# Kernel optimization log

Hardware: AMD Instinct MI355X
Metric: run time of the kernel (lower is better)

## Reference

```python
import jax, jax.numpy as jnp
import numpy as np

HIDDEN = 128   # hidden_dim == input_dim (embedding feeds LSTMCell directly)
OUT = 200000   # output_dim: item catalog size
T = 64         # num_timesteps
K = 50         # num_recommendations
HIST = 200     # length of user history x


def setup_inputs() -> dict:
    key = jax.random.key(0)
    ks = jax.random.split(key, 6)
    s = 0.02
    return {
        "x": jax.random.randint(ks[0], (HIST,), 1, OUT + 1),  # 1-indexed items
        "embed_table": jax.random.normal(ks[1], (OUT, HIDDEN), jnp.float32) * s,
        "W_ih": jax.random.normal(ks[2], (4 * HIDDEN, HIDDEN), jnp.float32) * s,
        "W_hh": jax.random.normal(ks[3], (4 * HIDDEN, HIDDEN), jnp.float32) * s,
        "b_ih": jnp.zeros((4 * HIDDEN,), jnp.float32),
        "b_hh": jnp.zeros((4 * HIDDEN,), jnp.float32),
        "W_out": jax.random.normal(ks[4], (OUT, HIDDEN), jnp.float32) * s,
        "b_out": jnp.zeros((OUT,), jnp.float32),
    }


def reference(x, embed_table, W_ih, W_hh, b_ih, b_hh, W_out, b_out):
    # Faithful translation of RecModel.forward with prev_a_hat=None, prev_feedback=None.
    def step(carry, i):
        h, c, mask, a_hat, feedback = carry
        # at i==0 the embedding input is forced to zeros (feedback starts at 0 anyway)
        emb = jnp.where(i > 0, embed_table[a_hat] * feedback.astype(jnp.float32), 0.0)
        # LSTMCell: gates order (input, forget, cell, output) as in torch
        gates = W_ih @ emb + b_ih + W_hh @ h + b_hh
        ig, fg, gg, og = jnp.split(gates, 4)
        c_new = jax.nn.sigmoid(fg) * c + jax.nn.sigmoid(ig) * jnp.tanh(gg)
        h_new = jax.nn.sigmoid(og) * jnp.tanh(c_new)
        probs = jax.nn.softmax(W_out @ h_new + b_out)  # Softmax(dim=0) on [OUT]
        masked = probs * mask
        _, top_items = jax.lax.top_k(masked, K)
        hit = jnp.isin(top_items + 1, x)               # x is 1-indexed
        any_hit = jnp.any(hit)
        first_hit = top_items[jnp.argmax(hit)]         # first intersecting item
        a_new = jnp.where(any_hit, first_hit, top_items[0]).astype(jnp.int32)
        fb_new = jnp.where(any_hit, 1, -1).astype(jnp.int32)
        mask_new = mask.at[a_new].set(0.0)
        return (h_new, c_new, mask_new, a_new, fb_new), (a_new, fb_new, masked)

    init = (
        jnp.zeros((HIDDEN,), jnp.float32),
        jnp.zeros((HIDDEN,), jnp.float32),
        jnp.ones((OUT,), jnp.float32),
        jnp.array(0, jnp.int32),
        jnp.array(0, jnp.int32),
    )
    _, (a_hats, feedbacks, masked_probs) = jax.lax.scan(step, init, jnp.arange(T))
    return a_hats, feedbacks, masked_probs
```

## Files before the change

### kernel.cpp

```cpp
#include <hip/hip_runtime.h>
#include <stdint.h>

#define OUTN   200000
#define HID    128
#define NSTEP  64
#define KTOP   50
#define NBINS  1024
#define CAP    4096
#define NBLK   256
#define NTHR   512
#define NWRD   6250

__device__ __forceinline__ float dot128f(const float* __restrict__ w, const float* __restrict__ h){
  const float4* w4 = (const float4*)w;
  float acc = 0.f;
  #pragma unroll
  for (int k=0;k<32;k++){
    float4 q = w4[k];
    const float* hp = h + k*4;
    acc += q.x*hp[0] + q.y*hp[1] + q.z*hp[2] + q.w*hp[3];
  }
  return acc;
}

__device__ __forceinline__ int binOf(float l, float rlo, float rsc){
  float b = (l - rlo) * rsc;
  b = fminf(fmaxf(b, 0.f), (float)(NBINS-1));
  return (int)b;
}

__device__ __forceinline__ void blockRed5(float& mx, float& mn, float& a, float& b, float& c,
                                          int tid, float* sm ){
  #pragma unroll
  for (int o=32;o;o>>=1){
    mx=fmaxf(mx,__shfl_xor(mx,o)); mn=fminf(mn,__shfl_xor(mn,o));
    a+=__shfl_xor(a,o); b+=__shfl_xor(b,o); c+=__shfl_xor(c,o);
  }
  __syncthreads();
  if ((tid&63)==0){ int w=tid>>6; sm[w*5+0]=mx; sm[w*5+1]=mn; sm[w*5+2]=a; sm[w*5+3]=b; sm[w*5+4]=c; }
  __syncthreads();
  int nw = blockDim.x>>6;
  if (tid==0){
    for (int k=1;k<nw;k++){
      sm[0]=fmaxf(sm[0],sm[k*5+0]); sm[1]=fminf(sm[1],sm[k*5+1]);
      sm[2]+=sm[k*5+2]; sm[3]+=sm[k*5+3]; sm[4]+=sm[k*5+4];
    }
  }
  __syncthreads();
  mx=sm[0]; mn=sm[1]; a=sm[2]; b=sm[3]; c=sm[4];
}

__device__ __forceinline__ void blockRedPair(float& p, int& i, int tid, float* smp, int* smi){
  __syncthreads();
  #pragma unroll
  for (int o=32;o;o>>=1){
    float p2=__shfl_xor(p,o); int i2=__shfl_xor(i,o);
    if (p2>p || (p2==p && i2<i)){ p=p2; i=i2; }
  }
  if ((tid&63)==0){ smp[tid>>6]=p; smi[tid>>6]=i; }
  __syncthreads();
  if (tid==0){
    for (int k=1;k<8;k++){
      if (smp[k]>smp[0] || (smp[k]==smp[0] && smi[k]<smi[0])){ smp[0]=smp[k]; smi[0]=smi[k]; }
    }
  }
  __syncthreads();
  p=smp[0]; i=smi[0];
}

__device__ __forceinline__ int blockRedSum(int v, int tid, int* smi){
  __syncthreads();
  #pragma unroll
  for (int o=32;o;o>>=1) v += __shfl_xor(v,o);
  if ((tid&63)==0) smi[tid>>6]=v;
  __syncthreads();
  if (tid==0){ int s=0; for(int k=0;k<8;k++) s+=smi[k]; smi[0]=s; }
  __syncthreads();
  return smi[0];
}

__device__ __forceinline__ void histSelect(unsigned* histL, unsigned* csum, int tid, int K, int* outp){
  int base = NBINS - 2*(tid+1);
  csum[tid] = histL[base] + histL[base+1];
  __syncthreads();
  for (int off=1; off<NTHR; off<<=1){
    unsigned add = (tid>=off) ? csum[tid-off] : 0u;
    __syncthreads();
    csum[tid] += add;
    __syncthreads();
  }
  unsigned pre = (tid==0)?0u:csum[tid-1];
  if (csum[tid] >= (unsigned)K && pre < (unsigned)K){
    unsigned run = pre; int bs = base;
    for (int b=base+1; b>=base; --b){
      run += histL[b];
      if (run >= (unsigned)K){ bs=b; break; }
    }
    outp[0]=bs; outp[1]=(int)run;
  }
  __syncthreads();
}

extern "C" __global__ void k_init(const int* __restrict__ x,
                                  const float* __restrict__ b_ih, const float* __restrict__ b_hh,
                                  unsigned* mask_bits, unsigned* inx_bits, unsigned* hist_g,
                                  unsigned* gcount, float* rparams, float* h_ws, float* c_ws)
{
  int tid = threadIdx.x;
  for (int i=tid;i<NWRD;i+=1024){ mask_bits[i]=0xFFFFFFFFu; inx_bits[i]=0u; }
  for (int i=tid;i<NBINS;i+=1024) hist_g[i]=0u;
  if (tid==0){ *gcount=0u; rparams[0]=0.f; rparams[1]=0.f; }
  if (tid<HID){
    float ig=b_ih[tid]       +b_hh[tid];
    float gg=b_ih[tid+2*HID] +b_hh[tid+2*HID];
    float og=b_ih[tid+3*HID] +b_hh[tid+3*HID];
    float si=1.f/(1.f+expf(-ig)), so=1.f/(1.f+expf(-og));
    float cn=si*tanhf(gg);
    c_ws[tid]=cn; h_ws[tid]=so*tanhf(cn);
  }
  __syncthreads();
  if (tid<200){
    int v = x[tid]-1;
    if (v>=0 && v<OUTN) atomicOr(&inx_bits[v>>5], 1u<<(v&31));
  }
}

extern "C" __global__ void __launch_bounds__(NTHR) k_logits(
    const float* __restrict__ W_out, const float* __restrict__ b_out,
    const unsigned* __restrict__ mask_bits, const float* __restrict__ h_ws,
    const float* __restrict__ rparams,
    float* __restrict__ l_ws, unsigned* __restrict__ hist_g, float* __restrict__ partials)
{
  __shared__ float    h_l[HID];
  __shared__ unsigned hl[NBINS];
  __shared__ float    smf[48];
  int tid=threadIdx.x, bid=blockIdx.x;
  if (tid<HID) h_l[tid]=h_ws[tid];
  for (int i=tid;i<NBINS;i+=NTHR) hl[i]=0u;
  __syncthreads();
  const float rlo=rparams[0], rsc=rparams[1];
  int start = bid*781 + (bid<64 ? bid : 64);
  int cnt   = 781 + (bid<64 ? 1 : 0);
  float mx=-3e38f, mn=3e38f, se=0.f, sl=0.f, sl2=0.f;
  for (int j=tid;j<cnt;j+=NTHR){
    int row = start+j;
    float l = dot128f(W_out+(size_t)row*HID, h_l) + b_out[row];
    l_ws[row]=l;
    se += expf(l)-1.f; sl += l; sl2 += l*l;
    if ((mask_bits[row>>5]>>(row&31))&1u){
      mx=fmaxf(mx,l); mn=fminf(mn,l);
      atomicAdd(&hl[binOf(l,rlo,rsc)],1u);
    }
  }
  blockRed5(mx,mn,se,sl,sl2,tid,smf);
  if (tid==0){ float* p=&partials[bid*8]; p[0]=mx;p[1]=mn;p[2]=se;p[3]=sl;p[4]=sl2; }
  for (int i=tid;i<NBINS;i+=NTHR){ unsigned v=hl[i]; if (v) atomicAdd(&hist_g[i],v); }
}

extern "C" __global__ void __launch_bounds__(NTHR) k_emit(
    const float* __restrict__ l_ws, const unsigned* __restrict__ mask_bits,
    const unsigned* __restrict__ hist_g, const float* __restrict__ partials,
    const float* __restrict__ rparams,
    float* __restrict__ out, unsigned* __restrict__ cand, unsigned* __restrict__ gcount,
    int t)
{
  __shared__ unsigned hl[NBINS];
  __shared__ unsigned csum[NTHR];
  __shared__ float    smf[48];
  __shared__ int      s_sel[2];
  int tid=threadIdx.x, bid=blockIdx.x;
  float mx=-3e38f,mn=3e38f,se=0.f,sl=0.f,sl2=0.f;
  if (tid<NBLK){ const float* p=&partials[tid*8]; mx=p[0];mn=p[1];se=p[2];sl=p[3];sl2=p[4]; }
  for (int i=tid;i<NBINS;i+=NTHR) hl[i]=hist_g[i];
  blockRed5(mx,mn,se,sl,sl2,tid,smf);
  const float invS = 1.f/(2.0e5f + se);
  histSelect(hl,csum,tid,KTOP,s_sel);
  const int bstar=s_sel[0];
  const float rlo=rparams[0], rsc=rparams[1];
  const bool doComp = (s_sel[1]<=CAP) && (rsc>0.f);
  float* orow = out + 2*NSTEP + (size_t)t*OUTN;
  int start = bid*781 + (bid<64 ? bid : 64);
  int cnt   = 781 + (bid<64 ? 1 : 0);
  for (int j=tid;j<cnt;j+=NTHR){
    int row = start+j;
    float l = l_ws[row];
    bool m = (mask_bits[row>>5]>>(row&31))&1u;
    orow[row] = m ? expf(l)*invS : 0.f;
    if (doComp && m && binOf(l,rlo,rsc)>=bstar){
      unsigned pos = atomicAdd(gcount,1u);
      if (pos<CAP) cand[pos]=(unsigned)row;
    }
  }
}

extern "C" __global__ void __launch_bounds__(NTHR) k_select(
    const float* __restrict__ emb_t,
    const float* __restrict__ W_ih, const float* __restrict__ W_hh,
    const float* __restrict__ b_ih, const float* __restrict__ b_hh,
    const float* __restrict__ l_ws, const float* __restrict__ partials,
    unsigned* mask_bits, const unsigned* __restrict__ inx_bits,
    unsigned* hist_g, unsigned* cand, unsigned* gcount,
    float* rparams, float* h_ws, float* c_ws,
    float* __restrict__ out, int t)
{
  __shared__ unsigned hl[NBINS];
  __shared__ unsigned csum[NTHR];
  __shared__ float    smf[48];
  __shared__ float    smp[8];
  __shared__ int      smi[8];
  __shared__ int      s_sel[2];
  __shared__ int      s_nc, s_cnt;
  __shared__ float    emb_l[HID], h_l[HID], gates[4*HID];
  int tid=threadIdx.x;

  float mx=-3e38f,mn=3e38f,se=0.f,sl=0.f,sl2=0.f;
  if (tid<NBLK){ const float* p=&partials[tid*8]; mx=p[0];mn=p[1];se=p[2];sl=p[3];sl2=p[4]; }
  for (int i=tid;i<NBINS;i+=NTHR) hl[i]=hist_g[i];
  blockRed5(mx,mn,se,sl,sl2,tid,smf);
  const float gmax=mx, gmin=mn, slg=sl, sl2g=sl2;
  histSelect(hl,csum,tid,KTOP,s_sel);
  const float rsc=rparams[1];
  const bool doComp = (s_sel[1]<=CAP) && (rsc>0.f);
  int nc = doComp ? (int)*gcount : 0;
  bool ok = doComp && nc>=KTOP && nc<=CAP;

  if (!ok){
    if (gmin >= gmax){
      if (tid==0){
        int c=0;
        for (int i=0;i<OUTN && c<KTOP;i++)
          if ((mask_bits[i>>5]>>(i&31))&1u) cand[c++]=(unsigned)i;
        s_nc=c;
      }
    } else {
      for (int i=tid;i<NBINS;i+=NTHR) hl[i]=0u;
      __syncthreads();
      const float sc2 = (float)NBINS/(gmax-gmin);
      for (int i=tid;i<OUTN;i+=NTHR)
        if ((mask_bits[i>>5]>>(i&31))&1u)
          atomicAdd(&hl[binOf(l_ws[i],gmin,sc2)],1u);
      __syncthreads();
      histSelect(hl,csum,tid,KTOP,s_sel);
      int b2=s_sel[0], c2=s_sel[1];
      if (c2<=CAP){
        if (tid==0) s_cnt=0;
        __syncthreads();
        for (int i=tid;i<OUTN;i+=NTHR){
          if ((mask_bits[i>>5]>>(i&31))&1u && binOf(l_ws[i],gmin,sc2)>=b2){
            int p=atomicAdd(&s_cnt,1);
            if (p<CAP) cand[p]=(unsigned)i;
          }
        }
        __syncthreads();
        if (tid==0) s_nc = (s_cnt<CAP ? s_cnt : CAP);
      } else {
        if (tid==0){
          int c=0;
          for (int i=0;i<OUTN && c<KTOP;i++)
            if (((mask_bits[i>>5]>>(i&31))&1u) && binOf(l_ws[i],gmin,sc2)>=b2) cand[c++]=(unsigned)i;
          s_nc=c;
        }
      }
    }
    __syncthreads();
    nc = s_nc;
  }

  float bp=-3.4e38f; int bi=0x7fffffff;
  float hp=-3.4e38f; int hidx=0x7fffffff;
  for (int j=tid;j<nc;j+=NTHR){
    int idx=(int)cand[j];
    float l=l_ws[idx];
    if (l>bp || (l==bp && idx<bi)){ bp=l; bi=idx; }
    if (((inx_bits[idx>>5]>>(idx&31))&1u) && (l>hp || (l==hp && idx<hidx))){ hp=l; hidx=idx; }
  }
  blockRedPair(bp,bi,tid,smp,smi);
  blockRedPair(hp,hidx,tid,smp,smi);
  int a, fb;
  if (hidx != 0x7fffffff){
    int cnt=0;
    for (int j=tid;j<nc;j+=NTHR){
      int idx=(int)cand[j];
      float l=l_ws[idx];
      cnt += (l>hp || (l==hp && idx<hidx)) ? 1 : 0;
    }
    cnt = blockRedSum(cnt,tid,smi);
    if (cnt < KTOP){ a=hidx; fb=1; } else { a=bi; fb=-1; }
  } else { a=bi; fb=-1; }
  if (a<0 || a>=OUTN) a=0;

  if (tid==0){
    out[t]       = (float)a;
    out[NSTEP+t] = (float)fb;
    atomicAnd(&mask_bits[a>>5], ~(1u<<(a&31)));
  }

  if (tid<HID){
    h_l[tid]  = h_ws[tid];
    emb_l[tid]= emb_t[(size_t)a*HID+tid] * (float)fb;
  }
  __syncthreads();
  float g = dot128f(W_ih+(size_t)tid*HID, emb_l) + dot128f(W_hh+(size_t)tid*HID, h_l)
          + b_ih[tid] + b_hh[tid];
  gates[tid]=g;
  __syncthreads();
  if (tid<HID){
    float ig=gates[tid], fg=gates[tid+HID], gg=gates[tid+2*HID], og=gates[tid+3*HID];
    float si=1.f/(1.f+expf(-ig)), sf=1.f/(1.f+expf(-fg)), so=1.f/(1.f+expf(-og));
    float cn=sf*c_ws[tid]+si*tanhf(gg);
    float hn=so*tanhf(cn);
    c_ws[tid]=cn; h_ws[tid]=hn;
  }

  for (int i=tid;i<NBINS;i+=NTHR) hist_g[i]=0u;
  if (tid==0){
    *gcount=0u;
    float mean=slg/2.0e5f;
    float var =sl2g/2.0e5f - mean*mean;
    float sg  =sqrtf(fmaxf(var,0.f));
    rparams[0]=gmax-24.f*sg;
    rparams[1]=(sg>0.f)?((float)NBINS/(32.f*sg)):0.f;
  }
}

extern "C" void kernel_launch(void* const* d_in, const int* in_sizes, int n_in,
                              void* d_out, int out_size, void* d_ws, size_t ws_size,
                              hipStream_t stream)
{
  const int*   x    = (const int*)d_in[0];
  const float* emb  = (const float*)d_in[1];
  const float* Wih  = (const float*)d_in[2];
  const float* Whh  = (const float*)d_in[3];
  const float* bih  = (const float*)d_in[4];
  const float* bhh  = (const float*)d_in[5];
  const float* Wout = (const float*)d_in[6];
  const float* bout = (const float*)d_in[7];
  float* out = (float*)d_out;

  char* ws = (char*)d_ws;
  float*    l_ws      = (float*)(ws + 0);
  float*    partials  = (float*)(ws + 800000);
  unsigned* mask_bits = (unsigned*)(ws + 808192);
  unsigned* inx_bits  = (unsigned*)(ws + 833280);
  unsigned* hist_g    = (unsigned*)(ws + 858368);
  unsigned* cand      = (unsigned*)(ws + 862464);
  unsigned* gcount    = (unsigned*)(ws + 878848);
  float*    rparams   = (float*)(ws + 879104);
  float*    h_ws      = (float*)(ws + 879360);
  float*    c_ws      = (float*)(ws + 879872);

  hipLaunchKernelGGL(k_init, dim3(1), dim3(1024), 0, stream,
                     x, bih, bhh, mask_bits, inx_bits, hist_g, gcount, rparams, h_ws, c_ws);

  for (int t=0; t<NSTEP; ++t){
    hipLaunchKernelGGL(k_logits, dim3(NBLK), dim3(NTHR), 0, stream,
                       Wout, bout, mask_bits, h_ws, rparams, l_ws, hist_g, partials);
    hipLaunchKernelGGL(k_emit, dim3(NBLK), dim3(NTHR), 0, stream,
                       l_ws, mask_bits, hist_g, partials, rparams, out, cand, gcount, t);
    hipLaunchKernelGGL(k_select, dim3(1), dim3(NTHR), 0, stream,
                       emb, Wih, Whh, bih, bhh, l_ws, partials, mask_bits, inx_bits,
                       hist_g, cand, gcount, rparams, h_ws, c_ws, out, t);
  }
}
```

Before: 4.362 ms.

## Fuse per-step kernels into one persistent cooperative kernel with grid barriers

Replaces the three launches per timestep (logits, emit, select), 192 in total, with a single cooperative persistent kernel. Steps are separated by atomic-counter grid barriers, and block 0 does the serial selection and LSTM update. This removes launch overhead and inter-kernel gaps across the 64 steps. In exchange, 255 blocks spin idle while block 0 runs the serial select phase, and correctness depends on all 256 blocks being co-resident.

```diff
diff --git a/kernel.cpp b/kernel.cpp
--- a/kernel.cpp
+++ b/kernel.cpp
@@ -101,15 +101,31 @@
   __syncthreads();
 }
 
+__device__ __forceinline__ void gsync(unsigned* bar, unsigned target){
+  __syncthreads();
+  if (threadIdx.x==0){
+    __threadfence();
+    __hip_atomic_fetch_add(bar, 1u, __ATOMIC_RELAXED, __HIP_MEMORY_SCOPE_AGENT);
+    unsigned v;
+    do {
+      __builtin_amdgcn_s_sleep(4);
+      v = __hip_atomic_load(bar, __ATOMIC_RELAXED, __HIP_MEMORY_SCOPE_AGENT);
+    } while (v < target);
+    __threadfence();
+  }
+  __syncthreads();
+}
+
 extern "C" __global__ void k_init(const int* __restrict__ x,
                                   const float* __restrict__ b_ih, const float* __restrict__ b_hh,
                                   unsigned* mask_bits, unsigned* inx_bits, unsigned* hist_g,
-                                  unsigned* gcount, float* rparams, float* h_ws, float* c_ws)
+                                  unsigned* gcount, float* rparams, float* h_ws, float* c_ws,
+                                  unsigned* bar)
 {
   int tid = threadIdx.x;
   for (int i=tid;i<NWRD;i+=1024){ mask_bits[i]=0xFFFFFFFFu; inx_bits[i]=0u; }
   for (int i=tid;i<NBINS;i+=1024) hist_g[i]=0u;
-  if (tid==0){ *gcount=0u; rparams[0]=0.f; rparams[1]=0.f; }
+  if (tid==0){ *gcount=0u; rparams[0]=0.f; rparams[1]=0.f; *bar=0u; }
   if (tid<HID){
     float ig=b_ih[tid]       +b_hh[tid];
     float gg=b_ih[tid+2*HID] +b_hh[tid+2*HID];
@@ -125,84 +141,21 @@
   }
 }
 
-extern "C" __global__ void __launch_bounds__(NTHR) k_logits(
-    const float* __restrict__ W_out, const float* __restrict__ b_out,
-    const unsigned* __restrict__ mask_bits, const float* __restrict__ h_ws,
-    const float* __restrict__ rparams,
-    float* __restrict__ l_ws, unsigned* __restrict__ hist_g, float* __restrict__ partials)
+struct FusedP {
+  const float* emb;  const float* Wih;  const float* Whh;
+  const float* bih;  const float* bhh;  const float* Wout; const float* bout;
+  float* out;
+  float* l_ws; float* partials;
+  unsigned* mask_bits; unsigned* inx_bits; unsigned* hist_g;
+  unsigned* cand; unsigned* gcount; float* rparams;
+  float* h_ws; float* c_ws; unsigned* bar;
+};
+
+extern "C" __global__ void __launch_bounds__(NTHR) k_fused(FusedP p)
 {
   __shared__ float    h_l[HID];
-  __shared__ unsigned hl[NBINS];
-  __shared__ float    smf[48];
-  int tid=threadIdx.x, bid=blockIdx.x;
-  if (tid<HID) h_l[tid]=h_ws[tid];
-  for (int i=tid;i<NBINS;i+=NTHR) hl[i]=0u;
-  __syncthreads();
-  const float rlo=rparams[0], rsc=rparams[1];
-  int start = bid*781 + (bid<64 ? bid : 64);
-  int cnt   = 781 + (bid<64 ? 1 : 0);
-  float mx=-3e38f, mn=3e38f, se=0.f, sl=0.f, sl2=0.f;
-  for (int j=tid;j<cnt;j+=NTHR){
-    int row = start+j;
-    float l = dot128f(W_out+(size_t)row*HID, h_l) + b_out[row];
-    l_ws[row]=l;
-    se += expf(l)-1.f; sl += l; sl2 += l*l;
-    if ((mask_bits[row>>5]>>(row&31))&1u){
-      mx=fmaxf(mx,l); mn=fminf(mn,l);
-      atomicAdd(&hl[binOf(l,rlo,rsc)],1u);
-    }
-  }
-  blockRed5(mx,mn,se,sl,sl2,tid,smf);
-  if (tid==0){ float* p=&partials[bid*8]; p[0]=mx;p[1]=mn;p[2]=se;p[3]=sl;p[4]=sl2; }
-  for (int i=tid;i<NBINS;i+=NTHR){ unsigned v=hl[i]; if (v) atomicAdd(&hist_g[i],v); }
-}
-
-extern "C" __global__ void __launch_bounds__(NTHR) k_emit(
-    const float* __restrict__ l_ws, const unsigned* __restrict__ mask_bits,
-    const unsigned* __restrict__ hist_g, const float* __restrict__ partials,
-    const float* __restrict__ rparams,
-    float* __restrict__ out, unsigned* __restrict__ cand, unsigned* __restrict__ gcount,
-    int t)
-{
-  __shared__ unsigned hl[NBINS];
-  __shared__ unsigned csum[NTHR];
-  __shared__ float    smf[48];
-  __shared__ int      s_sel[2];
-  int tid=threadIdx.x, bid=blockIdx.x;
-  float mx=-3e38f,mn=3e38f,se=0.f,sl=0.f,sl2=0.f;
-  if (tid<NBLK){ const float* p=&partials[tid*8]; mx=p[0];mn=p[1];se=p[2];sl=p[3];sl2=p[4]; }
-  for (int i=tid;i<NBINS;i+=NTHR) hl[i]=hist_g[i];
-  blockRed5(mx,mn,se,sl,sl2,tid,smf);
-  const float invS = 1.f/(2.0e5f + se);
-  histSelect(hl,csum,tid,KTOP,s_sel);
-  const int bstar=s_sel[0];
-  const float rlo=rparams[0], rsc=rparams[1];
-  const bool doComp = (s_sel[1]<=CAP) && (rsc>0.f);
-  float* orow = out + 2*NSTEP + (size_t)t*OUTN;
-  int start = bid*781 + (bid<64 ? bid : 64);
-  int cnt   = 781 + (bid<64 ? 1 : 0);
-  for (int j=tid;j<cnt;j+=NTHR){
-    int row = start+j;
-    float l = l_ws[row];
-    bool m = (mask_bits[row>>5]>>(row&31))&1u;
-    orow[row] = m ? expf(l)*invS : 0.f;
-    if (doComp && m && binOf(l,rlo,rsc)>=bstar){
-      unsigned pos = atomicAdd(gcount,1u);
-      if (pos<CAP) cand[pos]=(unsigned)row;
-    }
-  }
-}
-
-extern "C" __global__ void __launch_bounds__(NTHR) k_select(
-    const float* __restrict__ emb_t,
-    const float* __restrict__ W_ih, const float* __restrict__ W_hh,
-    const float* __restrict__ b_ih, const float* __restrict__ b_hh,
-    const float* __restrict__ l_ws, const float* __restrict__ partials,
-    unsigned* mask_bits, const unsigned* __restrict__ inx_bits,
-    unsigned* hist_g, unsigned* cand, unsigned* gcount,
-    float* rparams, float* h_ws, float* c_ws,
-    float* __restrict__ out, int t)
-{
+  __shared__ float    emb_l[HID];
+  __shared__ float    gates[4*HID];
   __shared__ unsigned hl[NBINS];
   __shared__ unsigned csum[NTHR];
   __shared__ float    smf[48];
@@ -210,116 +163,179 @@
   __shared__ int      smi[8];
   __shared__ int      s_sel[2];
   __shared__ int      s_nc, s_cnt;
-  __shared__ float    emb_l[HID], h_l[HID], gates[4*HID];
-  int tid=threadIdx.x;
-
-  float mx=-3e38f,mn=3e38f,se=0.f,sl=0.f,sl2=0.f;
-  if (tid<NBLK){ const float* p=&partials[tid*8]; mx=p[0];mn=p[1];se=p[2];sl=p[3];sl2=p[4]; }
-  for (int i=tid;i<NBINS;i+=NTHR) hl[i]=hist_g[i];
-  blockRed5(mx,mn,se,sl,sl2,tid,smf);
-  const float gmax=mx, gmin=mn, slg=sl, sl2g=sl2;
-  histSelect(hl,csum,tid,KTOP,s_sel);
-  const float rsc=rparams[1];
-  const bool doComp = (s_sel[1]<=CAP) && (rsc>0.f);
-  int nc = doComp ? (int)*gcount : 0;
-  bool ok = doComp && nc>=KTOP && nc<=CAP;
-
-  if (!ok){
-    if (gmin >= gmax){
-      if (tid==0){
-        int c=0;
-        for (int i=0;i<OUTN && c<KTOP;i++)
-          if ((mask_bits[i>>5]>>(i&31))&1u) cand[c++]=(unsigned)i;
-        s_nc=c;
-      }
-    } else {
-      for (int i=tid;i<NBINS;i+=NTHR) hl[i]=0u;
-      __syncthreads();
-      const float sc2 = (float)NBINS/(gmax-gmin);
-      for (int i=tid;i<OUTN;i+=NTHR)
-        if ((mask_bits[i>>5]>>(i&31))&1u)
-          atomicAdd(&hl[binOf(l_ws[i],gmin,sc2)],1u);
-      __syncthreads();
-      histSelect(hl,csum,tid,KTOP,s_sel);
-      int b2=s_sel[0], c2=s_sel[1];
-      if (c2<=CAP){
-        if (tid==0) s_cnt=0;
+
+  const int tid=threadIdx.x, bid=blockIdx.x;
+  const int start = bid*781 + (bid<64 ? bid : 64);
+  const int cnt   = 781 + (bid<64 ? 1 : 0);
+  unsigned barT = 0;
+
+  for (int t=0; t<NSTEP; ++t){
+    if (tid<HID) h_l[tid]=p.h_ws[tid];
+    for (int i=tid;i<NBINS;i+=NTHR) hl[i]=0u;
+    float rlo = p.rparams[0], rsc = p.rparams[1];
+    __syncthreads();
+    float mx=-3e38f, mn=3e38f, se=0.f, sl=0.f, sl2=0.f;
+    for (int j=tid;j<cnt;j+=NTHR){
+      int row = start+j;
+      float l = dot128f(p.Wout+(size_t)row*HID, h_l) + p.bout[row];
+      p.l_ws[row]=l;
+      se += expf(l)-1.f; sl += l; sl2 += l*l;
+      if ((p.mask_bits[row>>5]>>(row&31))&1u){
+        mx=fmaxf(mx,l); mn=fminf(mn,l);
+        if (rsc>0.f) atomicAdd(&hl[binOf(l,rlo,rsc)],1u);
+      }
+    }
+    blockRed5(mx,mn,se,sl,sl2,tid,smf);
+    if (tid==0){ float* q=&p.partials[bid*8]; q[0]=mx;q[1]=mn;q[2]=se;q[3]=sl;q[4]=sl2; }
+    if (rsc>0.f){
+      for (int i=tid;i<NBINS;i+=NTHR){ unsigned v=hl[i]; if (v) atomicAdd(&p.hist_g[i],v); }
+    }
+    barT += NBLK; gsync(p.bar, barT);
+
+    if (!(rsc>0.f)){
+      float bmx=-3e38f,bmn=3e38f,bse=0.f,bsl=0.f,bsl2=0.f;
+      if (tid<NBLK){ const float* q=&p.partials[tid*8]; bmx=q[0];bmn=q[1];bse=q[2];bsl=q[3];bsl2=q[4]; }
+      blockRed5(bmx,bmn,bse,bsl,bsl2,tid,smf);
+      float mean=bsl/2.0e5f, var=bsl2/2.0e5f-mean*mean, sg=sqrtf(fmaxf(var,0.f));
+      rlo = bmx-24.f*sg; rsc = (sg>0.f)?((float)NBINS/(32.f*sg)):0.f;
+      if (rsc>0.f){
+        for (int i=tid;i<NBINS;i+=NTHR) hl[i]=0u;
         __syncthreads();
-        for (int i=tid;i<OUTN;i+=NTHR){
-          if ((mask_bits[i>>5]>>(i&31))&1u && binOf(l_ws[i],gmin,sc2)>=b2){
-            int p=atomicAdd(&s_cnt,1);
-            if (p<CAP) cand[p]=(unsigned)i;
+        for (int j=tid;j<cnt;j+=NTHR){
+          int row=start+j;
+          if ((p.mask_bits[row>>5]>>(row&31))&1u)
+            atomicAdd(&hl[binOf(p.l_ws[row],rlo,rsc)],1u);
+        }
+        __syncthreads();
+        for (int i=tid;i<NBINS;i+=NTHR){ unsigned v=hl[i]; if (v) atomicAdd(&p.hist_g[i],v); }
+      }
+      barT += NBLK; gsync(p.bar, barT);
+    }
+
+    float gmx=-3e38f,gmn=3e38f,gse=0.f,gsl=0.f,gsl2=0.f;
+    if (tid<NBLK){ const float* q=&p.partials[tid*8]; gmx=q[0];gmn=q[1];gse=q[2];gsl=q[3];gsl2=q[4]; }
+    for (int i=tid;i<NBINS;i+=NTHR) hl[i]=p.hist_g[i];
+    if (tid==0){ s_sel[0]=NBINS; s_sel[1]=0x7fffffff; }
+    blockRed5(gmx,gmn,gse,gsl,gsl2,tid,smf);
+    const float invS = 1.f/(2.0e5f + gse);
+    histSelect(hl,csum,tid,KTOP,s_sel);
+    const int  bstar  = s_sel[0];
+    const int  bcnt   = s_sel[1];
+    const bool doComp = (bcnt<=CAP) && (rsc>0.f);
+    float* orow = p.out + 2*NSTEP + (size_t)t*OUTN;
+    for (int j=tid;j<cnt;j+=NTHR){
+      int row = start+j;
+      float l = p.l_ws[row];
+      bool m = (p.mask_bits[row>>5]>>(row&31))&1u;
+      orow[row] = m ? expf(l)*invS : 0.f;
+      if (doComp && m && binOf(l,rlo,rsc)>=bstar){
+        unsigned pos = atomicAdd(p.gcount,1u);
+        if (pos<CAP) p.cand[pos]=(unsigned)row;
+      }
+    }
+    barT += NBLK; gsync(p.bar, barT);
+
+    if (bid==0){
+      int nc = doComp ? (int)(*p.gcount) : 0;
+      bool ok = doComp && nc>=KTOP && nc<=CAP;
+
+      if (!ok){
+        if (gmn >= gmx){
+          if (tid==0){
+            int c=0;
+            for (int i=0;i<OUTN && c<KTOP;i++)
+              if ((p.mask_bits[i>>5]>>(i&31))&1u) p.cand[c++]=(unsigned)i;
+            s_nc=c;
+          }
+        } else {
+          for (int i=tid;i<NBINS;i+=NTHR) hl[i]=0u;
+          __syncthreads();
+          const float sc2 = (float)NBINS/(gmx-gmn);
+          for (int i=tid;i<OUTN;i+=NTHR)
+            if ((p.mask_bits[i>>5]>>(i&31))&1u)
+              atomicAdd(&hl[binOf(p.l_ws[i],gmn,sc2)],1u);
+          __syncthreads();
+          histSelect(hl,csum,tid,KTOP,s_sel);
+          int b2=s_sel[0], c2=s_sel[1];
+          if (c2<=CAP){
+            if (tid==0) s_cnt=0;
+            __syncthreads();
+            for (int i=tid;i<OUTN;i+=NTHR){
+              if ((p.mask_bits[i>>5]>>(i&31))&1u && binOf(p.l_ws[i],gmn,sc2)>=b2){
+                int q=atomicAdd(&s_cnt,1);
+                if (q<CAP) p.cand[q]=(unsigned)i;
+              }
+            }
+            __syncthreads();
+            if (tid==0) s_nc = (s_cnt<CAP ? s_cnt : CAP);
+          } else {
+            if (tid==0){
+              int c=0;
+              for (int i=0;i<OUTN && c<KTOP;i++)
+                if (((p.mask_bits[i>>5]>>(i&31))&1u) && binOf(p.l_ws[i],gmn,sc2)>=b2) p.cand[c++]=(unsigned)i;
+              s_nc=c;
+            }
           }
         }
         __syncthreads();
-        if (tid==0) s_nc = (s_cnt<CAP ? s_cnt : CAP);
-      } else {
-        if (tid==0){
-          int c=0;
-          for (int i=0;i<OUTN && c<KTOP;i++)
-            if (((mask_bits[i>>5]>>(i&31))&1u) && binOf(l_ws[i],gmin,sc2)>=b2) cand[c++]=(unsigned)i;
-          s_nc=c;
+        nc = s_nc;
+      }
+
+      float bp=-3.4e38f; int bi=0x7fffffff;
+      float hp=-3.4e38f; int hidx=0x7fffffff;
+      for (int j=tid;j<nc;j+=NTHR){
+        int idx=(int)p.cand[j];
+        float l=p.l_ws[idx];
+        if (l>bp || (l==bp && idx<bi)){ bp=l; bi=idx; }
+        if (((p.inx_bits[idx>>5]>>(idx&31))&1u) && (l>hp || (l==hp && idx<hidx))){ hp=l; hidx=idx; }
+      }
+      blockRedPair(bp,bi,tid,smp,smi);
+      blockRedPair(hp,hidx,tid,smp,smi);
+      int a, fb;
+      if (hidx != 0x7fffffff){
+        int better=0;
+        for (int j=tid;j<nc;j+=NTHR){
+          int idx=(int)p.cand[j];
+          float l=p.l_ws[idx];
+          better += (l>hp || (l==hp && idx<hidx)) ? 1 : 0;
         }
-      }
-    }
-    __syncthreads();
-    nc = s_nc;
-  }
-
-  float bp=-3.4e38f; int bi=0x7fffffff;
-  float hp=-3.4e38f; int hidx=0x7fffffff;
-  for (int j=tid;j<nc;j+=NTHR){
-    int idx=(int)cand[j];
-    float l=l_ws[idx];
-    if (l>bp || (l==bp && idx<bi)){ bp=l; bi=idx; }
-    if (((inx_bits[idx>>5]>>(idx&31))&1u) && (l>hp || (l==hp && idx<hidx))){ hp=l; hidx=idx; }
-  }
-  blockRedPair(bp,bi,tid,smp,smi);
-  blockRedPair(hp,hidx,tid,smp,smi);
-  int a, fb;
-  if (hidx != 0x7fffffff){
-    int cnt=0;
-    for (int j=tid;j<nc;j+=NTHR){
-      int idx=(int)cand[j];
-      float l=l_ws[idx];
-      cnt += (l>hp || (l==hp && idx<hidx)) ? 1 : 0;
-    }
-    cnt = blockRedSum(cnt,tid,smi);
-    if (cnt < KTOP){ a=hidx; fb=1; } else { a=bi; fb=-1; }
-  } else { a=bi; fb=-1; }
-  if (a<0 || a>=OUTN) a=0;
-
-  if (tid==0){
-    out[t]       = (float)a;
-    out[NSTEP+t] = (float)fb;
-    atomicAnd(&mask_bits[a>>5], ~(1u<<(a&31)));
-  }
-
-  if (tid<HID){
-    h_l[tid]  = h_ws[tid];
-    emb_l[tid]= emb_t[(size_t)a*HID+tid] * (float)fb;
-  }
-  __syncthreads();
-  float g = dot128f(W_ih+(size_t)tid*HID, emb_l) + dot128f(W_hh+(size_t)tid*HID, h_l)
-          + b_ih[tid] + b_hh[tid];
-  gates[tid]=g;
-  __syncthreads();
-  if (tid<HID){
-    float ig=gates[tid], fg=gates[tid+HID], gg=gates[tid+2*HID], og=gates[tid+3*HID];
-    float si=1.f/(1.f+expf(-ig)), sf=1.f/(1.f+expf(-fg)), so=1.f/(1.f+expf(-og));
-    float cn=sf*c_ws[tid]+si*tanhf(gg);
-    float hn=so*tanhf(cn);
-    c_ws[tid]=cn; h_ws[tid]=hn;
-  }
-
-  for (int i=tid;i<NBINS;i+=NTHR) hist_g[i]=0u;
-  if (tid==0){
-    *gcount=0u;
-    float mean=slg/2.0e5f;
-    float var =sl2g/2.0e5f - mean*mean;
-    float sg  =sqrtf(fmaxf(var,0.f));
-    rparams[0]=gmax-24.f*sg;
-    rparams[1]=(sg>0.f)?((float)NBINS/(32.f*sg)):0.f;
+        better = blockRedSum(better,tid,smi);
+        if (better < KTOP){ a=hidx; fb=1; } else { a=bi; fb=-1; }
+      } else { a=bi; fb=-1; }
+      if (a<0 || a>=OUTN) a=0;
+
+      if (tid==0){
+        p.out[t]       = (float)a;
+        p.out[NSTEP+t] = (float)fb;
+        atomicAnd(&p.mask_bits[a>>5], ~(1u<<(a&31)));
+      }
+
+      if (tid<HID) emb_l[tid]=p.emb[(size_t)a*HID+tid] * (float)fb;
+      __syncthreads();
+      float g = dot128f(p.Wih+(size_t)tid*HID, emb_l) + dot128f(p.Whh+(size_t)tid*HID, h_l)
+              + p.bih[tid] + p.bhh[tid];
+      gates[tid]=g;
+      __syncthreads();
+      if (tid<HID){
+        float ig=gates[tid], fg=gates[tid+HID], gg=gates[tid+2*HID], og=gates[tid+3*HID];
+        float si=1.f/(1.f+expf(-ig)), sf=1.f/(1.f+expf(-fg)), so=1.f/(1.f+expf(-og));
+        float cn=sf*p.c_ws[tid]+si*tanhf(gg);
+        float hn=so*tanhf(cn);
+        p.c_ws[tid]=cn; p.h_ws[tid]=hn;
+      }
+
+      if (tid==0){
+        *p.gcount=0u;
+        float mean=gsl/2.0e5f;
+        float var =gsl2/2.0e5f - mean*mean;
+        float sg  =sqrtf(fmaxf(var,0.f));
+        p.rparams[0]=gmx-24.f*sg;
+        p.rparams[1]=(sg>0.f)?((float)NBINS/(32.f*sg)):0.f;
+      }
+    } else if (bid==1){
+      for (int i=tid;i<NBINS;i+=NTHR) p.hist_g[i]=0u;
+    }
+    barT += NBLK; gsync(p.bar, barT);
   }
 }
 
@@ -345,20 +361,21 @@
   unsigned* hist_g    = (unsigned*)(ws + 858368);
   unsigned* cand      = (unsigned*)(ws + 862464);
   unsigned* gcount    = (unsigned*)(ws + 878848);
+  unsigned* bar       = (unsigned*)(ws + 878976);
   float*    rparams   = (float*)(ws + 879104);
   float*    h_ws      = (float*)(ws + 879360);
   float*    c_ws      = (float*)(ws + 879872);
 
   hipLaunchKernelGGL(k_init, dim3(1), dim3(1024), 0, stream,
-                     x, bih, bhh, mask_bits, inx_bits, hist_g, gcount, rparams, h_ws, c_ws);
-
-  for (int t=0; t<NSTEP; ++t){
-    hipLaunchKernelGGL(k_logits, dim3(NBLK), dim3(NTHR), 0, stream,
-                       Wout, bout, mask_bits, h_ws, rparams, l_ws, hist_g, partials);
-    hipLaunchKernelGGL(k_emit, dim3(NBLK), dim3(NTHR), 0, stream,
-                       l_ws, mask_bits, hist_g, partials, rparams, out, cand, gcount, t);
-    hipLaunchKernelGGL(k_select, dim3(1), dim3(NTHR), 0, stream,
-                       emb, Wih, Whh, bih, bhh, l_ws, partials, mask_bits, inx_bits,
-                       hist_g, cand, gcount, rparams, h_ws, c_ws, out, t);
-  }
-}
+                     x, bih, bhh, mask_bits, inx_bits, hist_g, gcount, rparams, h_ws, c_ws, bar);
+
+  FusedP p;
+  p.emb=emb; p.Wih=Wih; p.Whh=Whh; p.bih=bih; p.bhh=bhh; p.Wout=Wout; p.bout=bout;
+  p.out=out; p.l_ws=l_ws; p.partials=partials;
+  p.mask_bits=mask_bits; p.inx_bits=inx_bits; p.hist_g=hist_g;
+  p.cand=cand; p.gcount=gcount; p.rparams=rparams;
+  p.h_ws=h_ws; p.c_ws=c_ws; p.bar=bar;
+
+  void* args[] = { &p };
+  hipLaunchCooperativeKernel((const void*)k_fused, dim3(NBLK), dim3(NTHR), args, 0, stream);
+}
```

Measured after the change: 6.064 ms. +39.0%, slower.
